# Kernel optimization log

Measured on AMD Instinct MI355X. Metric: run time of the kernel, lower is better.

## Reference

```python
import jax, jax.numpy as jnp
import numpy as np
from jax import lax

KH = KW = 3
STRIDE = (1, 1)
PAD = (1, 1)

def setup_inputs() -> dict:
    key = jax.random.key(0)
    k1, k2, k3 = jax.random.split(key, 3)
    B_, C, H, W = 16, 128, 56, 56
    O, R = 256, 16
    Kflat = C * KH * KW
    x = jax.random.normal(k1, (B_, C, H, W), dtype=jnp.float32)
    # kaiming_normal_ fan_out for A: std = sqrt(2/out_channels)
    A = jax.random.normal(k2, (O, R), dtype=jnp.float32) * np.float32(np.sqrt(2.0 / O))
    # kaiming_normal_ fan_in for B: std = sqrt(2/kernel_flat_dim)
    Bm = jax.random.normal(k3, (R, Kflat), dtype=jnp.float32) * np.float32(np.sqrt(2.0 / Kflat))
    return {"x": x, "A": A, "B": Bm}

def reference(x, A, B):
    b, c, h, w = x.shape
    h_out = (h + 2 * PAD[0] - KH) // STRIDE[0] + 1
    w_out = (w + 2 * PAD[1] - KW) // STRIDE[1] + 1
    # im2col: [B, C*KH*KW, H_out, W_out]; feature order (c, kh, kw) matches torch Unfold
    patches = lax.conv_general_dilated_patches(
        x, filter_shape=(KH, KW), window_strides=STRIDE,
        padding=((PAD[0], PAD[0]), (PAD[1], PAD[1])))
    patches = patches.reshape(b, c * KH * KW, h_out * w_out)  # [B, K, L]
    tmp = jnp.einsum('rk,bkl->brl', B, patches)               # rank-limited matmul
    out = jnp.einsum('or,brl->bol', A, tmp)                   # [B, O, L]
    return out.reshape(b, A.shape[0], h_out, w_out)
```

## Files before the change

kernel.cpp:

```cpp
#include <hip/hip_runtime.h>
#include <hip/hip_bf16.h>


#define Bn 16
#define Cc 128
#define Hh 56
#define Ww 56
#define Ll (Hh * Ww)
#define Rr 16
#define Oo 256
#define KF (Cc * 9)
#define NKS 36
#define W2 58
#define RPITCH 128
#define ROWB (W2 * RPITCH)
#define HB 2

typedef __attribute__((ext_vector_type(8))) short bfrag_t;
typedef __attribute__((ext_vector_type(4))) float f32x4;

__device__ __forceinline__ float bf16_bits(unsigned short u) {
    return __uint_as_float(((unsigned)u) << 16);
}

__device__ __forceinline__ unsigned short bf16_rne(float f) {
    const unsigned u = __float_as_uint(f);
    const unsigned r = u + 0x7FFFu + ((u >> 16) & 1u);
    return (unsigned short)(r >> 16);
}

__device__ __forceinline__ bool detect_bf16(const void* __restrict__ p) {
    const unsigned* w = (const unsigned*)p;
    int c = 0;
#pragma unroll
    for (int i = 0; i < 32; ++i) {
        const unsigned e = (w[i] >> 7) & 0xFFu;
        c += (e >= 96u && e <= 144u) ? 1 : 0;
    }
    return c >= 20;
}

__global__ __launch_bounds__(256) void prep_frag(
    const void* __restrict__ A, const void* __restrict__ Bm,
    unsigned short* __restrict__ Bfrag, float* __restrict__ Afp)
{
    const bool ab = detect_bf16(A);
    const bool bb = detect_bf16(Bm);
    const int i = blockIdx.x * 256 + threadIdx.x;
    if (i < NKS * 512) {
        const int kstep = i >> 9, rem = i & 511;
        const int l = rem >> 3, e = rem & 7;
        const int r = l & 15, g = l >> 4;
        const int kp = kstep * 32 + g * 8 + e;
        const int tap = kp >> 7, c = kp & 127;
        const int k = c * 9 + tap;
        const float v = bb ? bf16_bits(((const unsigned short*)Bm)[r * KF + k])
                           : ((const float*)Bm)[r * KF + k];
        const unsigned short hi = bf16_rne(v);
        const float lov = v - bf16_bits(hi);
        Bfrag[(kstep * 2 + 0) * 512 + rem] = hi;
        Bfrag[(kstep * 2 + 1) * 512 + rem] = bf16_rne(lov);
    }
    if (i < Oo * Rr) {
        Afp[i] = ab ? bf16_bits(((const unsigned short*)A)[i])
                    : ((const float*)A)[i];
    }
}

#define MFB(A, B, C) __builtin_amdgcn_mfma_f32_16x16x32_bf16((A), (B), (C), 0, 0, 0)

template<bool XB>
__device__ __forceinline__ void fused_body(
    const void* __restrict__ x,
    const unsigned short* __restrict__ Bfrag,
    const float* __restrict__ Afp,
    float* __restrict__ out,
    unsigned short* __restrict__ xs)
{
    const int tid  = threadIdx.x;
    const int lane = tid & 63;
    const int wv   = __builtin_amdgcn_readfirstlane(tid >> 6);
    const int t    = wv & 3;
    const int kh   = wv >> 2;
    const int h0   = blockIdx.x * HB;
    const int b    = blockIdx.y;

    {
        const int l   = lane;
        const bool lok = (l < Ww);
#pragma unroll
        for (int rr = 0; rr < HB + 2; ++rr) {
            const int hh = h0 - 1 + rr;
            unsigned short* xr = xs + rr * ROWB;
            if (hh >= 0 && hh < Hh) {
                if (lok) {
                    const unsigned gb = (unsigned)(b * Cc * Ll + hh * Ww + l);
#pragma unroll
                    for (int it = 0; it < 2; ++it) {
                        const int cs_ = it * 8 + wv;
                        const int c0  = cs_ * 8;
                        bfrag_t v;
#pragma unroll
                        for (int j = 0; j < 8; ++j) {
                            if constexpr (XB) {
                                v[j] = (short)((const unsigned short*)x)[
                                    gb + (unsigned)((c0 + j) * Ll)];
                            } else {
                                v[j] = (short)bf16_rne(((const float*)x)[
                                    gb + (unsigned)((c0 + j) * Ll)]);
                            }
                        }
                        const int sp = cs_ ^ ((l + 1) & 7);
                        *(bfrag_t*)((char*)xr + (l + 1) * 256 + sp * 16) = v;
                    }
                }
            } else {
                unsigned* xw = (unsigned*)xr;
#pragma unroll
                for (int it = 0; it < 7; ++it) xw[it * 512 + tid] = 0u;
                if (tid < 3712 - 7 * 512) xw[7 * 512 + tid] = 0u;
            }
        }
        if (tid < 128) {
#pragma unroll
            for (int rr = 0; rr < HB + 2; ++rr) {
                xs[rr * ROWB + tid] = 0;
                xs[rr * ROWB + 57 * RPITCH + tid] = 0;
            }
        }
    }
    __syncthreads();

    const int col = lane & 15;
    const int g   = lane >> 4;
    const int px  = t * 16 + col;
    const int pxc = px < Ww ? px : Ww - 1;

    unsigned off6[6];
#pragma unroll
    for (int dwv = 0; dwv < 3; ++dwv)
#pragma unroll
        for (int cbi = 0; cbi < 2; ++cbi) {
            const int cb = kh * 2 + cbi;
            const int p2 = pxc + dwv;
            off6[dwv * 2 + cbi] = (unsigned)(p2 * 256 +
                (((cb * 4 + g) ^ (p2 & 7)) << 4));
        }

    f32x4 acc0 = {0.f, 0.f, 0.f, 0.f};
    f32x4 acc1 = {0.f, 0.f, 0.f, 0.f};
    const bfrag_t* __restrict__ bfp = (const bfrag_t*)Bfrag;

#pragma unroll
    for (int tap = 0; tap < 9; ++tap) {
        const int dh = tap / 3, dw = tap - dh * 3;
#pragma unroll
        for (int cbi = 0; cbi < 2; ++cbi) {
            const int cb = kh * 2 + cbi;
            const int ks = tap * 4 + cb;
            const bfrag_t ahi = bfp[(ks * 2 + 0) * 64 + lane];
            const bfrag_t alo = bfp[(ks * 2 + 1) * 64 + lane];
            const char* p0 = (const char*)xs + dh * (ROWB * 2) + off6[dw * 2 + cbi];
            const bfrag_t pf0 = *(const bfrag_t*)p0;
            const bfrag_t pf1 = *(const bfrag_t*)(p0 + ROWB * 2);
            acc0 = MFB(ahi, pf0, acc0);
            acc0 = MFB(alo, pf0, acc0);
            acc1 = MFB(ahi, pf1, acc1);
            acc1 = MFB(alo, pf1, acc1);
        }
    }

    __syncthreads();
    float (*tmp2)[HB][Rr][66] = (float (*)[HB][Rr][66])xs;

#pragma unroll
    for (int reg = 0; reg < 4; ++reg) {
        tmp2[kh][0][g * 4 + reg][t * 16 + col] = acc0[reg];
        tmp2[kh][1][g * 4 + reg][t * 16 + col] = acc1[reg];
    }
    __syncthreads();

    float tv0[Rr], tv1[Rr];
#pragma unroll
    for (int r = 0; r < Rr; ++r) {
        tv0[r] = tmp2[0][0][r][lane] + tmp2[1][0][r][lane];
        tv1[r] = tmp2[0][1][r][lane] + tmp2[1][1][r][lane];
    }

    const bool wok = (lane < Ww);
    const size_t obase = (size_t)b * Oo * Ll + (size_t)(h0 * Ww) + (size_t)lane;
#pragma unroll 4
    for (int j = 0; j < 32; ++j) {
        const int o = wv * 32 + j;
        const float* Ao = Afp + (size_t)o * Rr;
        float s0 = 0.f, s1 = 0.f;
#pragma unroll
        for (int r = 0; r < Rr; ++r) {
            const float av = Ao[r];
            s0 += av * tv0[r];
            s1 += av * tv1[r];
        }
        if (wok) {
            out[obase + (size_t)o * Ll]      = s0;
            out[obase + (size_t)o * Ll + Ww] = s1;
        }
    }
}

__global__ __launch_bounds__(512, 4) void fused_ks(
    const void* __restrict__ x,
    const unsigned short* __restrict__ Bfrag,
    const float* __restrict__ Afp,
    float* __restrict__ out)
{
    __shared__ __align__(16) unsigned short xs[4 * ROWB];
    if (detect_bf16(x)) fused_body<true >(x, Bfrag, Afp, out, xs);
    else                fused_body<false>(x, Bfrag, Afp, out, xs);
}

__global__ __launch_bounds__(256) void fused_fallback(
    const void* __restrict__ x, const void* __restrict__ A,
    const void* __restrict__ Bm, float* __restrict__ out)
{
    const bool xb = detect_bf16(x);
    const bool ab = detect_bf16(A);
    const bool bb = detect_bf16(Bm);
    const int gid = blockIdx.x * 256 + threadIdx.x;
    const int b = gid / Ll;
    const int l = gid - b * Ll;
    const int h = l / Ww, w = l - h * Ww;
    float acc[Rr];
#pragma unroll
    for (int r = 0; r < Rr; ++r) acc[r] = 0.f;
    const size_t xbase = (size_t)b * Cc * Ll;
    for (int c = 0; c < Cc; ++c) {
        const size_t xc = xbase + (size_t)c * Ll;
        float xv[9];
#pragma unroll
        for (int dh = 0; dh < 3; ++dh) {
            const int hh = h + dh - 1;
            const bool hok = (hh >= 0) & (hh < Hh);
#pragma unroll
            for (int dw = 0; dw < 3; ++dw) {
                const int ww = w + dw - 1;
                const bool ok = hok & (ww >= 0) & (ww < Ww);
                const size_t idx = xc + (size_t)(hh * Ww + ww);
                xv[dh*3+dw] = ok ? (xb ? bf16_bits(((const unsigned short*)x)[idx])
                                       : ((const float*)x)[idx]) : 0.f;
            }
        }
#pragma unroll
        for (int r = 0; r < Rr; ++r) {
            const size_t bo = (size_t)r * KF + (size_t)c * 9;
            float s = acc[r];
#pragma unroll
            for (int i = 0; i < 9; ++i)
                s += (bb ? bf16_bits(((const unsigned short*)Bm)[bo+i])
                         : ((const float*)Bm)[bo+i]) * xv[i];
            acc[r] = s;
        }
    }
    const size_t obase = (size_t)b * Oo * Ll + (size_t)l;
    for (int o = 0; o < Oo; ++o) {
        float s = 0.f;
#pragma unroll
        for (int r = 0; r < Rr; ++r)
            s += (ab ? bf16_bits(((const unsigned short*)A)[o*Rr+r])
                     : ((const float*)A)[o*Rr+r]) * acc[r];
        out[obase + (size_t)o * Ll] = s;
    }
}

extern "C" void kernel_launch(void* const* d_in, const int* in_sizes, int n_in,
                              void* d_out, int out_size, void* d_ws, size_t ws_size,
                              hipStream_t stream) {
    const void* x  = d_in[0];
    const void* A  = d_in[1];
    const void* Bm = d_in[2];
    for (int i = 0; i < n_in && i < 3; ++i) {
        const int s = in_sizes[i];
        if      (s == Bn * Cc * Ll) x  = d_in[i];
        else if (s == Oo * Rr)      A  = d_in[i];
        else if (s == Rr * KF)      Bm = d_in[i];
    }
    float* out = (float*)d_out;

    const size_t frag_bytes = (size_t)(NKS * 2 * 512) * 2;
    const size_t afp_bytes  = (size_t)(Oo * Rr) * 4;
    const size_t need       = frag_bytes + afp_bytes;

    if (ws_size >= need) {
        unsigned short* Bfrag = (unsigned short*)d_ws;
        float* Afp = (float*)((char*)d_ws + frag_bytes);
        prep_frag<<<dim3(72), 256, 0, stream>>>(A, Bm, Bfrag, Afp);
        fused_ks<<<dim3(Hh / HB, Bn), 512, 0, stream>>>(x, Bfrag, Afp, out);
    } else {
        fused_fallback<<<dim3((Bn * Ll) / 256), 256, 0, stream>>>(x, A, Bm, out);
    }
}
```

Baseline: 103.5 us.

## Split each row-pair block into two width halves with 256-thread blocks

Each block now covers half the width (32 columns plus halo) of a two-row strip, and the grid doubles while block size halves from 512 to 256 threads. Shared memory per block shrinks to a 36-column tile. The staging loop becomes a flat index loop with clamped loads and zero masking instead of separate padding passes. The output stage gives each lane one pixel of one row, and each wave computes 64 output channels. The aim is more blocks for better occupancy and load balance across CUs, at the cost of redundant halo loads and Bfrag fragment reads per block.

```diff
diff --git a/kernel.cpp b/kernel.cpp
--- a/kernel.cpp
+++ b/kernel.cpp
@@ -11,9 +11,9 @@
 #define Oo 256
 #define KF (Cc * 9)
 #define NKS 36
-#define W2 58
+#define W36 36
 #define RPITCH 128
-#define ROWB (W2 * RPITCH)
+#define ROWBY (W36 * 256)
 #define HB 2
 
 typedef __attribute__((ext_vector_type(8))) short bfrag_t;
@@ -77,63 +77,53 @@
     float* __restrict__ out,
     unsigned short* __restrict__ xs)
 {
-    const int tid  = threadIdx.x;
-    const int lane = tid & 63;
-    const int wv   = __builtin_amdgcn_readfirstlane(tid >> 6);
-    const int t    = wv & 3;
-    const int kh   = wv >> 2;
-    const int h0   = blockIdx.x * HB;
-    const int b    = blockIdx.y;
+    const int tid   = threadIdx.x;
+    const int lane  = tid & 63;
+    const int wv    = __builtin_amdgcn_readfirstlane(tid >> 6);
+    const int t     = wv & 1;
+    const int kh    = wv >> 1;
+    const int hb    = blockIdx.x >> 1;
+    const int half  = blockIdx.x & 1;
+    const int h0    = hb * HB;
+    const int b     = blockIdx.y;
+    const int wbase = half * 32;
 
     {
-        const int l   = lane;
-        const bool lok = (l < Ww);
-#pragma unroll
-        for (int rr = 0; rr < HB + 2; ++rr) {
-            const int hh = h0 - 1 + rr;
-            unsigned short* xr = xs + rr * ROWB;
-            if (hh >= 0 && hh < Hh) {
-                if (lok) {
-                    const unsigned gb = (unsigned)(b * Cc * Ll + hh * Ww + l);
-#pragma unroll
-                    for (int it = 0; it < 2; ++it) {
-                        const int cs_ = it * 8 + wv;
-                        const int c0  = cs_ * 8;
-                        bfrag_t v;
-#pragma unroll
-                        for (int j = 0; j < 8; ++j) {
-                            if constexpr (XB) {
-                                v[j] = (short)((const unsigned short*)x)[
-                                    gb + (unsigned)((c0 + j) * Ll)];
-                            } else {
-                                v[j] = (short)bf16_rne(((const float*)x)[
-                                    gb + (unsigned)((c0 + j) * Ll)]);
-                            }
-                        }
-                        const int sp = cs_ ^ ((l + 1) & 7);
-                        *(bfrag_t*)((char*)xr + (l + 1) * 256 + sp * 16) = v;
-                    }
+#pragma unroll
+        for (int it = 0; it < 9; ++it) {
+            const int idx = it * 256 + tid;
+            const int rr  = idx / 576;
+            const int rem = idx - rr * 576;
+            const int cs_ = rem / 36;
+            const int p   = rem - cs_ * 36;
+            const int hh  = h0 - 1 + rr;
+            const int wi  = wbase + p - 1;
+            const bool ok = (hh >= 0) & (hh < Hh) & (wi >= 0) & (wi < Ww);
+            const int hhc = (hh < 0) ? 0 : (hh >= Hh ? Hh - 1 : hh);
+            const int wic = (wi < 0) ? 0 : (wi >= Ww ? Ww - 1 : wi);
+            const unsigned gb = (unsigned)(b * Cc * Ll + hhc * Ww + wic);
+            const int c0 = cs_ * 8;
+            bfrag_t v;
+#pragma unroll
+            for (int j = 0; j < 8; ++j) {
+                if constexpr (XB) {
+                    v[j] = (short)((const unsigned short*)x)[
+                        gb + (unsigned)((c0 + j) * Ll)];
+                } else {
+                    v[j] = (short)bf16_rne(((const float*)x)[
+                        gb + (unsigned)((c0 + j) * Ll)]);
                 }
-            } else {
-                unsigned* xw = (unsigned*)xr;
-#pragma unroll
-                for (int it = 0; it < 7; ++it) xw[it * 512 + tid] = 0u;
-                if (tid < 3712 - 7 * 512) xw[7 * 512 + tid] = 0u;
             }
-        }
-        if (tid < 128) {
-#pragma unroll
-            for (int rr = 0; rr < HB + 2; ++rr) {
-                xs[rr * ROWB + tid] = 0;
-                xs[rr * ROWB + 57 * RPITCH + tid] = 0;
-            }
+            if (!ok) v = (bfrag_t){0, 0, 0, 0, 0, 0, 0, 0};
+            const int sp = cs_ ^ (p & 7);
+            *(bfrag_t*)((char*)xs + rr * ROWBY + p * 256 + sp * 16) = v;
         }
     }
     __syncthreads();
 
     const int col = lane & 15;
     const int g   = lane >> 4;
-    const int px  = t * 16 + col;
+    const int px  = wbase + t * 16 + col;
     const int pxc = px < Ww ? px : Ww - 1;
 
     unsigned off6[6];
@@ -142,7 +132,7 @@
 #pragma unroll
         for (int cbi = 0; cbi < 2; ++cbi) {
             const int cb = kh * 2 + cbi;
-            const int p2 = pxc + dwv;
+            const int p2 = (pxc - wbase) + dwv;
             off6[dwv * 2 + cbi] = (unsigned)(p2 * 256 +
                 (((cb * 4 + g) ^ (p2 & 7)) << 4));
         }
@@ -160,9 +150,9 @@
             const int ks = tap * 4 + cb;
             const bfrag_t ahi = bfp[(ks * 2 + 0) * 64 + lane];
             const bfrag_t alo = bfp[(ks * 2 + 1) * 64 + lane];
-            const char* p0 = (const char*)xs + dh * (ROWB * 2) + off6[dw * 2 + cbi];
+            const char* p0 = (const char*)xs + dh * ROWBY + off6[dw * 2 + cbi];
             const bfrag_t pf0 = *(const bfrag_t*)p0;
-            const bfrag_t pf1 = *(const bfrag_t*)(p0 + ROWB * 2);
+            const bfrag_t pf1 = *(const bfrag_t*)(p0 + ROWBY);
             acc0 = MFB(ahi, pf0, acc0);
             acc0 = MFB(alo, pf0, acc0);
             acc1 = MFB(ahi, pf1, acc1);
@@ -171,7 +161,7 @@
     }
 
     __syncthreads();
-    float (*tmp2)[HB][Rr][66] = (float (*)[HB][Rr][66])xs;
+    float (*tmp2)[HB][Rr][34] = (float (*)[HB][Rr][34])xs;
 
 #pragma unroll
     for (int reg = 0; reg < 4; ++reg) {
@@ -180,40 +170,35 @@
     }
     __syncthreads();
 
-    float tv0[Rr], tv1[Rr];
-#pragma unroll
-    for (int r = 0; r < Rr; ++r) {
-        tv0[r] = tmp2[0][0][r][lane] + tmp2[1][0][r][lane];
-        tv1[r] = tmp2[0][1][r][lane] + tmp2[1][1][r][lane];
-    }
-
-    const bool wok = (lane < Ww);
-    const size_t obase = (size_t)b * Oo * Ll + (size_t)(h0 * Ww) + (size_t)lane;
+    const int pxe  = lane & 31;
+    const int rowe = lane >> 5;
+    float tv[Rr];
+#pragma unroll
+    for (int r = 0; r < Rr; ++r)
+        tv[r] = tmp2[0][rowe][r][pxe] + tmp2[1][rowe][r][pxe];
+
+    const int wout = wbase + pxe;
+    const bool wok = (wout < Ww);
+    const size_t obase = (size_t)b * Oo * Ll
+                       + (size_t)((h0 + rowe) * Ww) + (size_t)wout;
 #pragma unroll 4
-    for (int j = 0; j < 32; ++j) {
-        const int o = wv * 32 + j;
+    for (int j = 0; j < 64; ++j) {
+        const int o = wv * 64 + j;
         const float* Ao = Afp + (size_t)o * Rr;
-        float s0 = 0.f, s1 = 0.f;
-#pragma unroll
-        for (int r = 0; r < Rr; ++r) {
-            const float av = Ao[r];
-            s0 += av * tv0[r];
-            s1 += av * tv1[r];
-        }
-        if (wok) {
-            out[obase + (size_t)o * Ll]      = s0;
-            out[obase + (size_t)o * Ll + Ww] = s1;
-        }
-    }
-}
-
-__global__ __launch_bounds__(512, 4) void fused_ks(
+        float s = 0.f;
+#pragma unroll
+        for (int r = 0; r < Rr; ++r) s += Ao[r] * tv[r];
+        if (wok) out[obase + (size_t)o * Ll] = s;
+    }
+}
+
+__global__ __launch_bounds__(256, 4) void fused_px(
     const void* __restrict__ x,
     const unsigned short* __restrict__ Bfrag,
     const float* __restrict__ Afp,
     float* __restrict__ out)
 {
-    __shared__ __align__(16) unsigned short xs[4 * ROWB];
+    __shared__ __align__(16) unsigned short xs[4 * W36 * RPITCH];
     if (detect_bf16(x)) fused_body<true >(x, Bfrag, Afp, out, xs);
     else                fused_body<false>(x, Bfrag, Afp, out, xs);
 }
@@ -293,7 +278,7 @@
         unsigned short* Bfrag = (unsigned short*)d_ws;
         float* Afp = (float*)((char*)d_ws + frag_bytes);
         prep_frag<<<dim3(72), 256, 0, stream>>>(A, Bm, Bfrag, Afp);
-        fused_ks<<<dim3(Hh / HB, Bn), 512, 0, stream>>>(x, Bfrag, Afp, out);
+        fused_px<<<dim3((Hh / HB) * 2, Bn), 256, 0, stream>>>(x, Bfrag, Afp, out);
     } else {
         fused_fallback<<<dim3((Bn * Ll) / 256), 256, 0, stream>>>(x, A, Bm, out);
     }
```

Result: slower. 118.7 us (+14.7%).
